# Kernel optimization log

Hardware: AMD Instinct MI355X
Metric: run time of the kernel (lower is better)

Reference implementation:

```python
import jax, jax.numpy as jnp
import numpy as np

SEGMENT_LENGTHS = [2048, 4096, 8192]
DILATION_RATES = [1, 2, 4]
BATCH, SEQ_LEN, HEADS, HEAD_DIM = 1, 8192, 16, 64
SCALE = HEAD_DIM ** (-0.5)


def _hilbert_index_to_xy(index, n):
    # Exact replica of the torch module's integer Hilbert d->(x,y) mapping.
    x = y = 0
    s = 1
    while s < n:
        rx = 1 & (index // 2)
        ry = 1 & (index ^ rx)
        if ry == 0:
            if rx == 1:
                x, y = s - 1 - y, s - 1 - x
            x, y = y, x
        x += s * rx
        y += s * ry
        index //= 4
        s *= 2
    return x, y


def _hilbert_perm(n):
    # Replicates _generate_hilbert_indices, including the fill-in tail and
    d = 1
    while d * d < n:
        d *= 2
    idx = []
    for i in range(min(n, d * d)):
        x, y = _hilbert_index_to_xy(i, d)
        p = x * d + y
        if p < n:
            idx.append(p)
    if len(idx) < n:
        idx.extend(range(len(idx), n))
    perm = np.array(idx[:n], dtype=np.int64)
    inv = np.zeros(n, dtype=np.int64)
    inv[perm] = np.arange(n, dtype=np.int64)
    return perm, inv


_PERM_CACHE = {}


def _get_perm(n):
    if n not in _PERM_CACHE:
        _PERM_CACHE[n] = _hilbert_perm(n)
    return _PERM_CACHE[n]


def setup_inputs() -> dict:
    key = jax.random.key(0)
    kq, kk, kv = jax.random.split(key, 3)
    shape = (BATCH, SEQ_LEN, HEADS, HEAD_DIM)
    return {
        "q": jax.random.normal(kq, shape, dtype=jnp.float32),
        "k": jax.random.normal(kk, shape, dtype=jnp.float32),
        "v": jax.random.normal(kv, shape, dtype=jnp.float32),
    }


def reference(q, k, v) -> jnp.ndarray:
    B, L, H, D = q.shape
    n_groups = len(SEGMENT_LENGTHS)
    heads_per_group = max(1, H // n_groups)
    out = jnp.zeros_like(q)
    for g, (seg_len, dil) in enumerate(zip(SEGMENT_LENGTHS, DILATION_RATES)):
        S = min(seg_len, L)
        h0 = g * heads_per_group
        if h0 >= H:
            continue
        h1 = min(h0 + heads_per_group, H)
        assert L % S == 0, "seq_len must tile into segments"
        N = L // S  # number of segments
        Hg = h1 - h0
        # [B, N, S, Hg, D]
        qg = q[:, :, h0:h1].reshape(B, N, S, Hg, D)
        kg = k[:, :, h0:h1].reshape(B, N, S, Hg, D)
        vg = v[:, :, h0:h1].reshape(B, N, S, Hg, D)
        if S > 64:
            perm, inv = _get_perm(S)
        else:
            perm = np.arange(S, dtype=np.int64)
            inv = perm
        # dilation applied AFTER Hilbert ordering -> compose the gathers
        kv_idx = perm[np.arange(0, S, dil)]
        qp = qg[:, :, perm]           # [B,N,S,Hg,D]
        kd = kg[:, :, kv_idx]         # [B,N,S/dil,Hg,D]
        vd = vg[:, :, kv_idx]
        scores = jnp.einsum('bnqhd,bnkhd->bnhqk', qp, kd) * SCALE
        attn = jnp.nan_to_num(jax.nn.softmax(scores, axis=-1))
        og = jnp.einsum('bnhqk,bnkhd->bnqhd', attn, vd)  # [B,N,S,Hg,D]
        og = og[:, :, inv]            # inverse Hilbert scatter
        out = out.at[:, :, h0:h1].set(og.reshape(B, L, Hg, D))
    return out
```

## Files before the change

kernel.cpp:

```cpp
#include <hip/hip_runtime.h>
#include <hip/hip_bf16.h>

typedef __attribute__((ext_vector_type(8))) short bf16x8;
typedef __attribute__((ext_vector_type(4))) short s16x4;
typedef __attribute__((ext_vector_type(4))) float f32x4;

#define LDKP 72

__device__ __forceinline__ unsigned pk2(float a, float b) {
    union { __hip_bfloat162 h2; unsigned u; } c;
    c.h2 = __float22bfloat162_rn(make_float2(a, b));
    return c.u;
}

__device__ __forceinline__ void gld16(const void* g, void* l) {
    __builtin_amdgcn_global_load_lds(
        (const __attribute__((address_space(1))) unsigned*)g,
        (__attribute__((address_space(3))) unsigned*)l, 16, 0, 0);
}

__device__ inline int hilbert_p(int index, int d) {
    int x = 0, y = 0;
    for (int s = 1; s < d; s <<= 1) {
        int rx = (index >> 1) & 1;
        int ry = (index ^ rx) & 1;
        if (ry == 0) {
            if (rx == 1) {
                int nx = s - 1 - y;
                int ny = s - 1 - x;
                x = nx; y = ny;
            }
            int t = x; x = y; y = t;
        }
        x += s * rx;
        y += s * ry;
        index >>= 2;
    }
    return x * d + y;
}

__global__ __launch_bounds__(256) void gather_kv(
    const float* __restrict__ K, const float* __restrict__ V,
    short* __restrict__ Kp, short* __restrict__ Vp)
{
    __shared__ short vt[64 * LDKP];

    const int b = blockIdx.x;
    int g, rb;
    if (b < 640)      { g = 0; rb = b; }
    else if (b < 960) { g = 1; rb = b - 640; }
    else              { g = 2; rb = b - 960; }
    const int nseg   = 4 >> g;
    const int hl     = rb / (nseg * 32);
    const int r2     = rb - hl * (nseg * 32);
    const int seg    = r2 >> 5;
    const int kt     = r2 & 31;
    const int h      = g * 5 + hl;
    const int S      = 2048 << g;
    const int segrow = seg * S;
    const int dgrid  = (g == 2) ? 128 : 64;
    const size_t tile_s = (size_t)b * 4096;

    for (int it = threadIdx.x; it < 512; it += 256) {
        const int j  = it >> 3;
        const int c8 = it & 7;
        const int ii = kt * 64 + j;
        const int p  = (g == 0) ? ii : hilbert_p(ii << g, dgrid);
        const size_t src = ((size_t)((segrow + p) * 16 + h)) * 64 + c8 * 8;
        const float4* kp = (const float4*)(K + src);
        const float4* vp = (const float4*)(V + src);
        float4 k0 = kp[0], k1 = kp[1];
        float4 v0 = vp[0], v1 = vp[1];
        union { unsigned u[4]; bf16x8 v; } ck, cv;
        ck.u[0] = pk2(k0.x, k0.y); ck.u[1] = pk2(k0.z, k0.w);
        ck.u[2] = pk2(k1.x, k1.y); ck.u[3] = pk2(k1.z, k1.w);
        cv.u[0] = pk2(v0.x, v0.y); cv.u[1] = pk2(v0.z, v0.w);
        cv.u[2] = pk2(v1.x, v1.y); cv.u[3] = pk2(v1.z, v1.w);
        *(bf16x8*)&Kp[tile_s + j * 64 + ((c8 ^ (j & 7)) * 8)] = ck.v;
        *(bf16x8*)&vt[j * LDKP + ((c8 ^ (j >> 3)) * 8)] = cv.v;
    }
    __syncthreads();
    for (int it = threadIdx.x; it < 512; it += 256) {
        const int dd = it >> 3;
        const int k8 = it & 7;
        union { short s[8]; bf16x8 v; } o;
#pragma unroll
        for (int u = 0; u < 8; ++u)
            o.s[u] = vt[(k8 * 8 + u) * LDKP + (((dd >> 3) ^ k8) * 8) + (dd & 7)];
        *(bf16x8*)&Vp[tile_s + dd * 64 + ((k8 ^ (dd & 7)) * 8)] = o.v;
    }
}

__global__ __launch_bounds__(256, 4) void attn_kernel(
    const float* __restrict__ Q, float* __restrict__ O,
    const short* __restrict__ Kp, const short* __restrict__ Vp)
{
    __shared__ __align__(16) short ldsK[2][4096];
    __shared__ __align__(16) short ldsV[2][4096];
    __shared__ __align__(16) short ldsP[64 * 64];

    const int bx = blockIdx.x;
    const int g  = bx / 320;
    const int r  = bx - g * 320;
    const int hl = r >> 6;
    const int qb = r & 63;
    const int h  = g * 5 + hl;
    const int qglob = qb * 128;
    const int seg   = qb >> (4 + g);
    const int tile0 = ((g == 0) ? 0 : (g == 1) ? 640 : 960) + (hl * (4 >> g) + seg) * 32;

    const int tid  = threadIdx.x;
    const int wave = tid >> 6;
    const int lane = tid & 63;
    const int ln   = lane & 15;
    const int quad = lane >> 4;

    if (g == 0 && hl == 0) {
        const float4 z = make_float4(0.f, 0.f, 0.f, 0.f);
        for (int i = tid; i < 2048; i += 256) {
            int row = qglob + (i >> 4);
            ((float4*)O)[(size_t)(row * 16 + 15) * 16 + (i & 15)] = z;
        }
    }

    const float cs = 0.125f * 1.44269504088896f;
    bf16x8 qf[2][2];
#pragma unroll
    for (int m2 = 0; m2 < 2; ++m2) {
        int qrow = qglob + wave * 32 + m2 * 16 + ln;
        const float* qp = Q + ((size_t)(qrow * 16 + h)) * 64;
#pragma unroll
        for (int kh = 0; kh < 2; ++kh) {
            const float4* p4 = (const float4*)(qp + kh * 32 + quad * 8);
            float4 a = p4[0], b = p4[1];
            union { unsigned u[4]; bf16x8 v; } f;
            f.u[0] = pk2(a.x * cs, a.y * cs); f.u[1] = pk2(a.z * cs, a.w * cs);
            f.u[2] = pk2(b.x * cs, b.y * cs); f.u[3] = pk2(b.z * cs, b.w * cs);
            qf[m2][kh] = f.v;
        }
    }

    f32x4 oacc[2][4];
#pragma unroll
    for (int a = 0; a < 2; ++a)
#pragma unroll
        for (int b = 0; b < 4; ++b)
            oacc[a][b] = (f32x4){0.f, 0.f, 0.f, 0.f};
    float lp[2] = {0.f, 0.f};

    const int prow_base = (wave * 16 + ln) * 64;
    const int lnx = ln & 7;

    {
        const size_t tb = (size_t)tile0 << 13;
        const char* kgp = (const char*)Kp + tb + (wave << 11) + (lane << 4);
        const char* vgp = (const char*)Vp + tb + (wave << 11) + (lane << 4);
        char* klp = (char*)&ldsK[0][0] + (wave << 11);
        char* vlp = (char*)&ldsV[0][0] + (wave << 11);
        gld16(kgp,        klp);
        gld16(kgp + 1024, klp + 1024);
        gld16(vgp,        vlp);
        gld16(vgp + 1024, vlp + 1024);
    }

    for (int kt = 0; kt < 32; ++kt) {
        const int cur = kt & 1;
        if (kt < 31) {
            const size_t tb = (size_t)(tile0 + kt + 1) << 13;
            const char* kgp = (const char*)Kp + tb + (wave << 11) + (lane << 4);
            const char* vgp = (const char*)Vp + tb + (wave << 11) + (lane << 4);
            char* klp = (char*)&ldsK[cur ^ 1][0] + (wave << 11);
            char* vlp = (char*)&ldsV[cur ^ 1][0] + (wave << 11);
            gld16(kgp,        klp);
            gld16(kgp + 1024, klp + 1024);
            gld16(vgp,        vlp);
            gld16(vgp + 1024, vlp + 1024);
            asm volatile("s_waitcnt vmcnt(4)" ::: "memory");
        } else {
            asm volatile("s_waitcnt vmcnt(0)" ::: "memory");
        }
        asm volatile("s_barrier" ::: "memory");

        const short* lK = ldsK[cur];
        const short* lV = ldsV[cur];

        bf16x8 kf[4][2];
#pragma unroll
        for (int kg = 0; kg < 4; ++kg)
#pragma unroll
            for (int kh = 0; kh < 2; ++kh)
                kf[kg][kh] = *(const bf16x8*)&lK[(kg * 16 + ln) * 64 + (((kh * 4 + quad) ^ lnx) * 8)];

        __builtin_amdgcn_s_setprio(1);
        {
            float lacc = 0.f;
#pragma unroll
            for (int kg = 0; kg < 4; ++kg) {
                f32x4 st = (f32x4){0.f, 0.f, 0.f, 0.f};
                st = __builtin_amdgcn_mfma_f32_16x16x32_bf16(kf[kg][0], qf[0][0], st, 0, 0, 0);
                st = __builtin_amdgcn_mfma_f32_16x16x32_bf16(kf[kg][1], qf[0][1], st, 0, 0, 0);
                float p0 = __builtin_amdgcn_exp2f(st[0]);
                float p1 = __builtin_amdgcn_exp2f(st[1]);
                float p2 = __builtin_amdgcn_exp2f(st[2]);
                float p3 = __builtin_amdgcn_exp2f(st[3]);
                lacc += (p0 + p1) + (p2 + p3);
                union { unsigned u[2]; s16x4 s; } pc;
                pc.u[0] = pk2(p0, p1); pc.u[1] = pk2(p2, p3);
                *(s16x4*)&ldsP[prow_base + (((kg * 2 + (quad >> 1)) ^ lnx) * 8) + (quad & 1) * 4] = pc.s;
            }
            lp[0] += lacc;
        }

        unsigned pc1[8];
        {
            float lacc = 0.f;
#pragma unroll
            for (int kg = 0; kg < 4; ++kg) {
                f32x4 st = (f32x4){0.f, 0.f, 0.f, 0.f};
                st = __builtin_amdgcn_mfma_f32_16x16x32_bf16(kf[kg][0], qf[1][0], st, 0, 0, 0);
                st = __builtin_amdgcn_mfma_f32_16x16x32_bf16(kf[kg][1], qf[1][1], st, 0, 0, 0);
                float p0 = __builtin_amdgcn_exp2f(st[0]);
                float p1 = __builtin_amdgcn_exp2f(st[1]);
                float p2 = __builtin_amdgcn_exp2f(st[2]);
                float p3 = __builtin_amdgcn_exp2f(st[3]);
                lacc += (p0 + p1) + (p2 + p3);
                pc1[kg * 2]     = pk2(p0, p1);
                pc1[kg * 2 + 1] = pk2(p2, p3);
            }
            lp[1] += lacc;
        }
        __builtin_amdgcn_s_setprio(0);

        __builtin_amdgcn_sched_barrier(0);

        bf16x8 vf[4][2];
#pragma unroll
        for (int n4 = 0; n4 < 4; ++n4)
#pragma unroll
            for (int kh = 0; kh < 2; ++kh)
                vf[n4][kh] = *(const bf16x8*)&lV[(n4 * 16 + ln) * 64 + (((kh * 4 + quad) ^ lnx) * 8)];

        bf16x8 ap0 = *(const bf16x8*)&ldsP[prow_base + ((quad ^ lnx) * 8)];
        bf16x8 ap1 = *(const bf16x8*)&ldsP[prow_base + (((4 + quad) ^ lnx) * 8)];
        __builtin_amdgcn_s_setprio(1);
#pragma unroll
        for (int n4 = 0; n4 < 4; ++n4) {
            oacc[0][n4] = __builtin_amdgcn_mfma_f32_16x16x32_bf16(ap0, vf[n4][0], oacc[0][n4], 0, 0, 0);
            oacc[0][n4] = __builtin_amdgcn_mfma_f32_16x16x32_bf16(ap1, vf[n4][1], oacc[0][n4], 0, 0, 0);
        }
        __builtin_amdgcn_s_setprio(0);

#pragma unroll
        for (int kg = 0; kg < 4; ++kg) {
            union { unsigned u[2]; s16x4 s; } w;
            w.u[0] = pc1[kg * 2]; w.u[1] = pc1[kg * 2 + 1];
            *(s16x4*)&ldsP[prow_base + (((kg * 2 + (quad >> 1)) ^ lnx) * 8) + (quad & 1) * 4] = w.s;
        }
        bf16x8 bp0 = *(const bf16x8*)&ldsP[prow_base + ((quad ^ lnx) * 8)];
        bf16x8 bp1 = *(const bf16x8*)&ldsP[prow_base + (((4 + quad) ^ lnx) * 8)];
        __builtin_amdgcn_s_setprio(1);
#pragma unroll
        for (int n4 = 0; n4 < 4; ++n4) {
            oacc[1][n4] = __builtin_amdgcn_mfma_f32_16x16x32_bf16(bp0, vf[n4][0], oacc[1][n4], 0, 0, 0);
            oacc[1][n4] = __builtin_amdgcn_mfma_f32_16x16x32_bf16(bp1, vf[n4][1], oacc[1][n4], 0, 0, 0);
        }
        __builtin_amdgcn_s_setprio(0);

        asm volatile("s_barrier" ::: "memory");
    }

    lp[0] += __shfl_xor(lp[0], 16, 64);
    lp[0] += __shfl_xor(lp[0], 32, 64);
    lp[1] += __shfl_xor(lp[1], 16, 64);
    lp[1] += __shfl_xor(lp[1], 32, 64);

#pragma unroll
    for (int m2 = 0; m2 < 2; ++m2) {
#pragma unroll
        for (int rg = 0; rg < 4; ++rg) {
            float lv  = __shfl(lp[m2], quad * 4 + rg, 64);
            float inv = 1.0f / lv;
            int qrow = qglob + wave * 32 + m2 * 16 + quad * 4 + rg;
            float* op = O + ((size_t)(qrow * 16 + h)) * 64;
#pragma unroll
            for (int n4 = 0; n4 < 4; ++n4)
                op[n4 * 16 + ln] = oacc[m2][n4][rg] * inv;
        }
    }
}

extern "C" void kernel_launch(void* const* d_in, const int* in_sizes, int n_in,
                              void* d_out, int out_size, void* d_ws, size_t ws_size,
                              hipStream_t stream) {
    const float* q = (const float*)d_in[0];
    const float* k = (const float*)d_in[1];
    const float* v = (const float*)d_in[2];
    float* out = (float*)d_out;
    short* Kp = (short*)d_ws;
    short* Vp = Kp + (size_t)1120 * 4096;

    gather_kv<<<1120, 256, 0, stream>>>(k, v, Kp, Vp);
    attn_kernel<<<960, 256, 0, stream>>>(q, out, Kp, Vp);
}
```

Before: 205.4 us.

## Load K/V MFMA fragments directly from global memory instead of LDS staging

Removes the double-buffered global_load_lds staging of K and V tiles and the per-iteration barriers. Each wave now reads its MFMA fragments straight from the preprocessed bf16 K/V buffers in global memory, which are written unswizzled to match the new access pattern. This frees LDS and removes synchronisation, but every wave reloads the same tile from global/L2 and there is no explicit prefetch, so load latency is exposed.

```diff
diff --git a/kernel.cpp b/kernel.cpp
--- a/kernel.cpp
+++ b/kernel.cpp
@@ -11,12 +11,6 @@
     union { __hip_bfloat162 h2; unsigned u; } c;
     c.h2 = __float22bfloat162_rn(make_float2(a, b));
     return c.u;
-}
-
-__device__ __forceinline__ void gld16(const void* g, void* l) {
-    __builtin_amdgcn_global_load_lds(
-        (const __attribute__((address_space(1))) unsigned*)g,
-        (__attribute__((address_space(3))) unsigned*)l, 16, 0, 0);
 }
 
 __device__ inline int hilbert_p(int index, int d) {
@@ -76,7 +70,7 @@
         ck.u[2] = pk2(k1.x, k1.y); ck.u[3] = pk2(k1.z, k1.w);
         cv.u[0] = pk2(v0.x, v0.y); cv.u[1] = pk2(v0.z, v0.w);
         cv.u[2] = pk2(v1.x, v1.y); cv.u[3] = pk2(v1.z, v1.w);
-        *(bf16x8*)&Kp[tile_s + j * 64 + ((c8 ^ (j & 7)) * 8)] = ck.v;
+        *(bf16x8*)&Kp[tile_s + j * 64 + c8 * 8] = ck.v;
         *(bf16x8*)&vt[j * LDKP + ((c8 ^ (j >> 3)) * 8)] = cv.v;
     }
     __syncthreads();
@@ -87,7 +81,7 @@
 #pragma unroll
         for (int u = 0; u < 8; ++u)
             o.s[u] = vt[(k8 * 8 + u) * LDKP + (((dd >> 3) ^ k8) * 8) + (dd & 7)];
-        *(bf16x8*)&Vp[tile_s + dd * 64 + ((k8 ^ (dd & 7)) * 8)] = o.v;
+        *(bf16x8*)&Vp[tile_s + dd * 64 + k8 * 8] = o.v;
     }
 }
 
@@ -95,8 +89,6 @@
     const float* __restrict__ Q, float* __restrict__ O,
     const short* __restrict__ Kp, const short* __restrict__ Vp)
 {
-    __shared__ __align__(16) short ldsK[2][4096];
-    __shared__ __align__(16) short ldsV[2][4096];
     __shared__ __align__(16) short ldsP[64 * 64];
 
     const int bx = blockIdx.x;
@@ -150,46 +142,18 @@
 
     const int prow_base = (wave * 16 + ln) * 64;
     const int lnx = ln & 7;
-
-    {
-        const size_t tb = (size_t)tile0 << 13;
-        const char* kgp = (const char*)Kp + tb + (wave << 11) + (lane << 4);
-        const char* vgp = (const char*)Vp + tb + (wave << 11) + (lane << 4);
-        char* klp = (char*)&ldsK[0][0] + (wave << 11);
-        char* vlp = (char*)&ldsV[0][0] + (wave << 11);
-        gld16(kgp,        klp);
-        gld16(kgp + 1024, klp + 1024);
-        gld16(vgp,        vlp);
-        gld16(vgp + 1024, vlp + 1024);
-    }
+    const int fo = ln * 64 + quad * 8;
 
     for (int kt = 0; kt < 32; ++kt) {
-        const int cur = kt & 1;
-        if (kt < 31) {
-            const size_t tb = (size_t)(tile0 + kt + 1) << 13;
-            const char* kgp = (const char*)Kp + tb + (wave << 11) + (lane << 4);
-            const char* vgp = (const char*)Vp + tb + (wave << 11) + (lane << 4);
-            char* klp = (char*)&ldsK[cur ^ 1][0] + (wave << 11);
-            char* vlp = (char*)&ldsV[cur ^ 1][0] + (wave << 11);
-            gld16(kgp,        klp);
-            gld16(kgp + 1024, klp + 1024);
-            gld16(vgp,        vlp);
-            gld16(vgp + 1024, vlp + 1024);
-            asm volatile("s_waitcnt vmcnt(4)" ::: "memory");
-        } else {
-            asm volatile("s_waitcnt vmcnt(0)" ::: "memory");
-        }
-        asm volatile("s_barrier" ::: "memory");
-
-        const short* lK = ldsK[cur];
-        const short* lV = ldsV[cur];
+        const short* kTile = Kp + ((size_t)(tile0 + kt) << 12);
+        const short* vTile = Vp + ((size_t)(tile0 + kt) << 12);
 
         bf16x8 kf[4][2];
 #pragma unroll
         for (int kg = 0; kg < 4; ++kg)
 #pragma unroll
             for (int kh = 0; kh < 2; ++kh)
-                kf[kg][kh] = *(const bf16x8*)&lK[(kg * 16 + ln) * 64 + (((kh * 4 + quad) ^ lnx) * 8)];
+                kf[kg][kh] = *(const bf16x8*)&kTile[fo + kg * 1024 + kh * 32];
 
         __builtin_amdgcn_s_setprio(1);
         {
@@ -238,7 +202,7 @@
         for (int n4 = 0; n4 < 4; ++n4)
 #pragma unroll
             for (int kh = 0; kh < 2; ++kh)
-                vf[n4][kh] = *(const bf16x8*)&lV[(n4 * 16 + ln) * 64 + (((kh * 4 + quad) ^ lnx) * 8)];
+                vf[n4][kh] = *(const bf16x8*)&vTile[fo + n4 * 1024 + kh * 32];
 
         bf16x8 ap0 = *(const bf16x8*)&ldsP[prow_base + ((quad ^ lnx) * 8)];
         bf16x8 ap1 = *(const bf16x8*)&ldsP[prow_base + (((4 + quad) ^ lnx) * 8)];
@@ -265,8 +229,6 @@
             oacc[1][n4] = __builtin_amdgcn_mfma_f32_16x16x32_bf16(bp1, vf[n4][1], oacc[1][n4], 0, 0, 0);
         }
         __builtin_amdgcn_s_setprio(0);
-
-        asm volatile("s_barrier" ::: "memory");
     }
 
     lp[0] += __shfl_xor(lp[0], 16, 64);
```

Result: slower. 353.8 us (+72.3%).
